# Optimization experiments

Measured on AMD Instinct MI355X. Metric: run time of the kernel, lower is better.

Reference implementation:

```python
import jax, jax.numpy as jnp
import numpy as np

H = 64  # hidden_size
B, S, DIN = 256, 4096, 1
NUM_LAYERS = 3


def setup_inputs() -> dict:
    key = jax.random.key(0)
    ks = jax.random.split(key, 32)
    s = 1.0 / np.sqrt(H)  # torch LSTM/Linear init bound
    inp = {"x": jax.random.normal(ks[0], (B, S, DIN), dtype=jnp.float32)}
    ki = 1
    for l in range(NUM_LAYERS):
        din = DIN if l == 0 else H
        inp[f"Wih{l}"] = jax.random.uniform(ks[ki], (4 * H, din), minval=-s, maxval=s); ki += 1
        inp[f"Whh{l}"] = jax.random.uniform(ks[ki], (4 * H, H), minval=-s, maxval=s); ki += 1
        inp[f"bih{l}"] = jax.random.uniform(ks[ki], (4 * H,), minval=-s, maxval=s); ki += 1
        inp[f"bhh{l}"] = jax.random.uniform(ks[ki], (4 * H,), minval=-s, maxval=s); ki += 1
    inp["Wlin"] = jax.random.uniform(ks[ki], (1, H), minval=-s, maxval=s); ki += 1
    inp["blin"] = jax.random.uniform(ks[ki], (1,), minval=-s, maxval=s)
    return inp


def _lstm_layer(x, Wih, Whh, bih, bhh):
    """x: [B,S,Din] -> (hs [B,S,H], h_T [B,H], c_T [B,H]). PyTorch gate order i,f,g,o."""
    # precompute input contribution for all timesteps (one big GEMM)
    xg = jnp.einsum('bsd,gd->bsg', x, Wih) + (bih + bhh)  # [B,S,4H]
    b = x.shape[0]
    h0 = jnp.zeros((b, H), x.dtype)
    c0 = jnp.zeros((b, H), x.dtype)

    def step(carry, xg_t):
        h, c = carry
        g = xg_t + h @ Whh.T  # [B,4H]
        i, f, gg, o = jnp.split(g, 4, axis=-1)
        c = jax.nn.sigmoid(f) * c + jax.nn.sigmoid(i) * jnp.tanh(gg)
        h = jax.nn.sigmoid(o) * jnp.tanh(c)
        return (h, c), h

    (hT, cT), hs = jax.lax.scan(step, (h0, c0), jnp.swapaxes(xg, 0, 1))
    return jnp.swapaxes(hs, 0, 1), hT, cT


def reference(x, Wih0, Whh0, bih0, bhh0, Wih1, Whh1, bih1, bhh1,
              Wih2, Whh2, bih2, bhh2, Wlin, blin):
    layers = [(Wih0, Whh0, bih0, bhh0), (Wih1, Whh1, bih1, bhh1), (Wih2, Whh2, bih2, bhh2)]
    out = x
    hTs, cTs = [], []
    for (Wih, Whh, bih, bhh) in layers:
        out, hT, cT = _lstm_layer(out, Wih, Whh, bih, bhh)
        hTs.append(hT); cTs.append(cT)
    y = out @ Wlin.T + blin  # [B,S,1]
    h_n = jnp.stack(hTs, axis=0)  # [num_layers,B,H]
    c_n = jnp.stack(cTs, axis=0)
    return y, h_n, c_n
```

## Files before the change

### kernel.cpp

```cpp
#include <hip/hip_runtime.h>
#include <stdint.h>


#define SQ 4096
#define HH 64
#define NB 256
#define WSEG 2048
#define WMAT 8192

typedef _Float16 h2  __attribute__((ext_vector_type(2)));
typedef uint32_t uv8 __attribute__((ext_vector_type(8)));

__device__ __forceinline__ h2 bch2(uint32_t u) { return __builtin_bit_cast(h2, u); }

template<int CTRL>
__device__ __forceinline__ float fdpp(float v) {
    return __builtin_bit_cast(float,
        __builtin_amdgcn_mov_dpp(__builtin_bit_cast(int, v), CTRL, 0xF, 0xF, true));
}
#define DPP_XOR1 0xB1
#define DPP_XOR2 0x4E
#define DPP_XOR3 0x1B
#define DPP_ROR4 0x124
#define DPP_ROR8 0x128

__device__ __forceinline__ float frcp(float x)  { return __builtin_amdgcn_rcpf(x); }
__device__ __forceinline__ float fexp2(float x) { return __builtin_amdgcn_exp2f(x); }

__device__ __forceinline__ uv8 load_pk(const uint32_t* __restrict__ p) {
    const uint4 a = *reinterpret_cast<const uint4*>(p);
    const uint4 b = *reinterpret_cast<const uint4*>(p + 4);
    uv8 r;
    r[0] = a.x; r[1] = a.y; r[2] = a.z; r[3] = a.w;
    r[4] = b.x; r[5] = b.y; r[6] = b.z; r[7] = b.w;
    return r;
}

__device__ __forceinline__ void pin(uv8& r) {
#pragma unroll
    for (int j = 0; j < 8; ++j) {
        uint32_t t = r[j];
        asm volatile("" : "+v"(t));
        r[j] = t;
    }
}

__device__ __forceinline__ float dotseg(uv8 w, uint4 a, uint4 b, float acc) {
    acc = __builtin_amdgcn_fdot2(bch2(w[0]), bch2(a.x), acc, false);
    acc = __builtin_amdgcn_fdot2(bch2(w[1]), bch2(a.y), acc, false);
    acc = __builtin_amdgcn_fdot2(bch2(w[2]), bch2(a.z), acc, false);
    acc = __builtin_amdgcn_fdot2(bch2(w[3]), bch2(a.w), acc, false);
    acc = __builtin_amdgcn_fdot2(bch2(w[4]), bch2(b.x), acc, false);
    acc = __builtin_amdgcn_fdot2(bch2(w[5]), bch2(b.y), acc, false);
    acc = __builtin_amdgcn_fdot2(bch2(w[6]), bch2(b.z), acc, false);
    acc = __builtin_amdgcn_fdot2(bch2(w[7]), bch2(b.w), acc, false);
    return acc;
}

__global__ __launch_bounds__(256)
void prep_weights(const float* __restrict__ Whh0, const float* __restrict__ Wih1,
                  const float* __restrict__ Whh1, const float* __restrict__ Wih2,
                  const float* __restrict__ Whh2, uint32_t* __restrict__ ws)
{
    const int idx = blockIdx.x * 256 + threadIdx.x;
    const int j   = idx & 7;
    const int k   = (idx >> 3) & 255;
    const int i   = (idx >> 11) & 3;
    const int mat = idx >> 13;
    const int u = k >> 2, qt = k & 3;
    const int row = ((qt ^ i) << 6) + u;
    const int col = (qt << 4) + (j << 1);
    const float* M = (mat == 0) ? Whh0 : (mat == 1) ? Wih1
                   : (mat == 2) ? Whh1 : (mat == 3) ? Wih2 : Whh2;
    h2 t;
    t[0] = (_Float16)M[row * HH + col];
    t[1] = (_Float16)M[row * HH + col + 1];
    ws[idx] = __builtin_bit_cast(uint32_t, t);
}

__global__ __launch_bounds__(768)
__attribute__((amdgpu_waves_per_eu(1, 3)))
void lstm3_fused(
    const float* __restrict__ x,
    const float* __restrict__ Wih0,
    const float* __restrict__ bih0, const float* __restrict__ bhh0,
    const float* __restrict__ bih1, const float* __restrict__ bhh1,
    const float* __restrict__ bih2, const float* __restrict__ bhh2,
    const float* __restrict__ Wlin, const float* __restrict__ blin,
    const uint32_t* __restrict__ wpk,
    float* __restrict__ out)
{
    const int b   = blockIdx.x;
    const int tid = threadIdx.x;
    const int grp = tid >> 8;
    const int k   = tid & 255;
    const int u   = k >> 2;
    const int qt  = k & 3;
    const int row = qt * HH + u;

    __shared__ __align__(16) float xrow[SQ];
    __shared__ __align__(16) uint4 hbf[2][3][8];
    __shared__ __align__(16) float ybuf[2][16];

    for (int i = tid; i < SQ; i += 768) xrow[i] = x[b * SQ + i];
    if (tid < 48) ((uint4*)hbf)[tid] = make_uint4(0, 0, 0, 0);
    if (tid < 32) ((float*)ybuf)[tid] = 0.f;

    const int matA = (grp == 0) ? 0 : (grp == 1) ? 1 : 3;
    const int matB = (grp == 1) ? 2 : 4;
    const uint32_t* pWA = wpk + matA * WMAT + k * 8;
    uv8 wA0 = load_pk(pWA + 0 * WSEG);
    uv8 wA1 = load_pk(pWA + 1 * WSEG);
    uv8 wA2 = load_pk(pWA + 2 * WSEG);
    uv8 wA3 = load_pk(pWA + 3 * WSEG);
    pin(wA0); pin(wA1); pin(wA2); pin(wA3);
    uv8 wB0 = {}, wB1 = {}, wB2 = {}, wB3 = {};
    if (grp != 0) {
        const uint32_t* pWB = wpk + matB * WMAT + k * 8;
        wB0 = load_pk(pWB + 0 * WSEG);
        wB1 = load_pk(pWB + 1 * WSEG);
        wB2 = load_pk(pWB + 2 * WSEG);
        wB3 = load_pk(pWB + 3 * WSEG);
        pin(wB0); pin(wB1); pin(wB2); pin(wB3);
    }

    float bias = 0.f, wih0 = 0.f, wlin_u = 0.f;
    if (grp == 0) { bias = bih0[row] + bhh0[row]; wih0 = Wih0[row]; }
    else if (grp == 1) bias = bih1[row] + bhh1[row];
    else { bias = bih2[row] + bhh2[row]; if (qt == 0) wlin_u = Wlin[u]; }
    const float blin_v = blin[0];

    const int la = (grp == 2) ? 1 : 0;
    const int lb = grp;
    const uint4* pA[2] = { &hbf[0][la][2 * qt], &hbf[1][la][2 * qt] };
    const uint4* pB[2] = { &hbf[0][lb][2 * qt], &hbf[1][lb][2 * qt] };
    _Float16* pW[2] = { (_Float16*)&hbf[0][grp][0] + u, (_Float16*)&hbf[1][grp][0] + u };

    const float s1  = (qt == 2) ? 2.f : 1.f;
    const float o1  = (qt == 2) ? 1.f : 0.f;
    const float ms1 = -s1 * 1.44269504f;
    float cc = 0.f;

    __syncthreads();

    auto tick = [&](int T, int rd) {
        const int wr = rd ^ 1;

        const uint4 a0 = pA[rd][0], a1 = pA[rd][1];
        float p0 = dotseg(wA0, a0, a1, 0.f);
        float p1 = dotseg(wA1, a0, a1, 0.f);
        float p2 = dotseg(wA2, a0, a1, 0.f);
        float p3 = dotseg(wA3, a0, a1, 0.f);
        if (grp != 0) {
            const uint4 c0 = pB[rd][0], c1 = pB[rd][1];
            p0 = dotseg(wB0, c0, c1, p0);
            p1 = dotseg(wB1, c0, c1, p1);
            p2 = dotseg(wB2, c0, c1, p2);
            p3 = dotseg(wB3, c0, c1, p3);
        }

        float g = (p0 + fdpp<DPP_XOR1>(p1))
                + fdpp<DPP_XOR2>(p2 + fdpp<DPP_XOR1>(p3));
        g += bias;
        if (grp == 0) g += wih0 * xrow[(T < SQ) ? T : 0];

        const float t   = frcp(1.f + fexp2(ms1 * g));
        const float act = s1 * t - o1;
        const float v1 = fdpp<DPP_XOR1>(act);
        const float v2 = fdpp<DPP_XOR2>(act);
        const float v3 = fdpp<DPP_XOR3>(act);

        const int step = T - grp;
        float yv = 0.f;
        if (qt == 0 && step >= 0 && step < SQ) {
            cc = v1 * cc + act * v2;
            float tc = fminf(fmaxf(cc, -15.f), 15.f);
            float e  = fexp2(tc * -2.88539008f);
            float h  = v3 * ((1.f - e) * frcp(1.f + e));
            *pW[wr] = (_Float16)h;
            if (grp == 2) yv = wlin_u * h;
            if (step == SQ - 1) {
                out[NB * SQ + grp * NB * HH + b * HH + u] = h;
                out[NB * SQ + 3 * NB * HH + grp * NB * HH + b * HH + u] = cc;
            }
        }
        if (grp == 2) {
            yv += fdpp<DPP_XOR1>(yv);
            yv += fdpp<DPP_XOR2>(yv);
            yv += fdpp<DPP_ROR4>(yv);
            yv += fdpp<DPP_ROR8>(yv);
            if ((k & 15) == 0) ybuf[rd][k >> 4] = yv;
        }
        if (grp == 0 && u == HH - 1) {
            const int sy = T - 3;
            if (sy >= 0 && sy < SQ) {
                const float4 v = ((const float4*)ybuf[rd ^ 1])[qt];
                float s = (v.x + v.y) + (v.z + v.w);
                s += fdpp<DPP_XOR1>(s);
                s += fdpp<DPP_XOR2>(s);
                if (qt == 3) out[b * SQ + sy] = s + blin_v;
            }
        }
        __syncthreads();
    };

    for (int T = 0; T < SQ + 4; T += 2) {
        tick(T, 0);
        tick(T + 1, 1);
    }
}

extern "C" void kernel_launch(void* const* d_in, const int* in_sizes, int n_in,
                              void* d_out, int out_size, void* d_ws, size_t ws_size,
                              hipStream_t stream) {
    const float* x    = (const float*)d_in[0];
    const float* Wih0 = (const float*)d_in[1];
    const float* Whh0 = (const float*)d_in[2];
    const float* bih0 = (const float*)d_in[3];
    const float* bhh0 = (const float*)d_in[4];
    const float* Wih1 = (const float*)d_in[5];
    const float* Whh1 = (const float*)d_in[6];
    const float* bih1 = (const float*)d_in[7];
    const float* bhh1 = (const float*)d_in[8];
    const float* Wih2 = (const float*)d_in[9];
    const float* Whh2 = (const float*)d_in[10];
    const float* bih2 = (const float*)d_in[11];
    const float* bhh2 = (const float*)d_in[12];
    const float* Wlin = (const float*)d_in[13];
    const float* blin = (const float*)d_in[14];
    float* out = (float*)d_out;

    uint32_t* wpk = (uint32_t*)d_ws;
    prep_weights<<<160, 256, 0, stream>>>(Whh0, Wih1, Whh1, Wih2, Whh2, wpk);
    lstm3_fused<<<NB, 768, 0, stream>>>(x, Wih0, bih0, bhh0,
                                        bih1, bhh1, bih2, bhh2,
                                        Wlin, blin, wpk, out);
}
```

Before: 2.894 ms.

## Compute recurrent LSTM matvecs with MFMA 16x16x32 instead of fdot2 chains

Replaces the per-lane fdot2 dot-product chains and DPP cross-lane gate reduction with MFMA 16x16x32 f16 instructions. The weights are repacked into MFMA A-fragment layout, and the h vector is broadcast as the B operand, so only one output column is meaningful. Results are scattered to a new LDS gate buffer by one lane per 16, then read back per gate row. This trades many VALU dot instructions for matrix-core ops plus an extra LDS round trip on the per-step critical path. It also wastes 15 of the 16 MFMA columns.

```diff
diff --git a/kernel.cpp b/kernel.cpp
--- a/kernel.cpp
+++ b/kernel.cpp
@@ -5,13 +5,10 @@
 #define SQ 4096
 #define HH 64
 #define NB 256
-#define WSEG 2048
-#define WMAT 8192
-
-typedef _Float16 h2  __attribute__((ext_vector_type(2)));
-typedef uint32_t uv8 __attribute__((ext_vector_type(8)));
-
-__device__ __forceinline__ h2 bch2(uint32_t u) { return __builtin_bit_cast(h2, u); }
+
+typedef _Float16 h2    __attribute__((ext_vector_type(2)));
+typedef _Float16 f16x8 __attribute__((ext_vector_type(8)));
+typedef float    f32x4 __attribute__((ext_vector_type(4)));
 
 template<int CTRL>
 __device__ __forceinline__ float fdpp(float v) {
@@ -27,34 +24,13 @@
 __device__ __forceinline__ float frcp(float x)  { return __builtin_amdgcn_rcpf(x); }
 __device__ __forceinline__ float fexp2(float x) { return __builtin_amdgcn_exp2f(x); }
 
-__device__ __forceinline__ uv8 load_pk(const uint32_t* __restrict__ p) {
-    const uint4 a = *reinterpret_cast<const uint4*>(p);
-    const uint4 b = *reinterpret_cast<const uint4*>(p + 4);
-    uv8 r;
-    r[0] = a.x; r[1] = a.y; r[2] = a.z; r[3] = a.w;
-    r[4] = b.x; r[5] = b.y; r[6] = b.z; r[7] = b.w;
-    return r;
-}
-
-__device__ __forceinline__ void pin(uv8& r) {
-#pragma unroll
-    for (int j = 0; j < 8; ++j) {
-        uint32_t t = r[j];
-        asm volatile("" : "+v"(t));
-        r[j] = t;
-    }
-}
-
-__device__ __forceinline__ float dotseg(uv8 w, uint4 a, uint4 b, float acc) {
-    acc = __builtin_amdgcn_fdot2(bch2(w[0]), bch2(a.x), acc, false);
-    acc = __builtin_amdgcn_fdot2(bch2(w[1]), bch2(a.y), acc, false);
-    acc = __builtin_amdgcn_fdot2(bch2(w[2]), bch2(a.z), acc, false);
-    acc = __builtin_amdgcn_fdot2(bch2(w[3]), bch2(a.w), acc, false);
-    acc = __builtin_amdgcn_fdot2(bch2(w[4]), bch2(b.x), acc, false);
-    acc = __builtin_amdgcn_fdot2(bch2(w[5]), bch2(b.y), acc, false);
-    acc = __builtin_amdgcn_fdot2(bch2(w[6]), bch2(b.z), acc, false);
-    acc = __builtin_amdgcn_fdot2(bch2(w[7]), bch2(b.w), acc, false);
-    return acc;
+__device__ __forceinline__ void pin4(uint4& r) {
+    asm volatile("" : "+v"(r.x), "+v"(r.y), "+v"(r.z), "+v"(r.w));
+}
+
+__device__ __forceinline__ f32x4 mm(uint4 wv, uint4 bv, f32x4 c) {
+    return __builtin_amdgcn_mfma_f32_16x16x32_f16(
+        __builtin_bit_cast(f16x8, wv), __builtin_bit_cast(f16x8, bv), c, 0, 0, 0);
 }
 
 __global__ __launch_bounds__(256)
@@ -63,19 +39,29 @@
                   const float* __restrict__ Whh2, uint32_t* __restrict__ ws)
 {
     const int idx = blockIdx.x * 256 + threadIdx.x;
-    const int j   = idx & 7;
-    const int k   = (idx >> 3) & 255;
-    const int i   = (idx >> 11) & 3;
-    const int mat = idx >> 13;
-    const int u = k >> 2, qt = k & 3;
-    const int row = ((qt ^ i) << 6) + u;
-    const int col = (qt << 4) + (j << 1);
-    const float* M = (mat == 0) ? Whh0 : (mat == 1) ? Wih1
-                   : (mat == 2) ? Whh1 : (mat == 3) ? Wih2 : Whh2;
-    h2 t;
-    t[0] = (_Float16)M[row * HH + col];
-    t[1] = (_Float16)M[row * HH + col + 1];
-    ws[idx] = __builtin_bit_cast(uint32_t, t);
+    int r, KT;
+    const float *Wi = nullptr, *Wh;
+    if (idx < 8192)       { r = idx;         KT = 2; Wh = Whh0; }
+    else if (idx < 24576) { r = idx - 8192;  KT = 4; Wi = Wih1; Wh = Whh1; }
+    else                  { r = idx - 24576; KT = 4; Wi = Wih2; Wh = Whh2; }
+    const int j   = r & 3;
+    const int l   = (r >> 2) & 63;
+    const int rem = r >> 8;
+    const int kt  = rem & (KT - 1);
+    const int tw  = rem / KT;
+    const int t   = tw & 3;
+    const int w   = tw >> 2;
+    const int p    = w * 64 + t * 16 + (l & 15);
+    const int orow = (p & 3) * 64 + (p >> 2);
+    const int kk   = (l >> 4) * 8 + 2 * j;
+    const float* M; int col;
+    if (KT == 2)     { M = Wh; col = kt * 32 + kk; }
+    else if (kt < 2) { M = Wi; col = kt * 32 + kk; }
+    else             { M = Wh; col = (kt - 2) * 32 + kk; }
+    h2 tt;
+    tt[0] = (_Float16)M[orow * HH + col];
+    tt[1] = (_Float16)M[orow * HH + col + 1];
+    ws[idx] = __builtin_bit_cast(uint32_t, tt);
 }
 
 __global__ __launch_bounds__(768)
@@ -97,31 +83,38 @@
     const int u   = k >> 2;
     const int qt  = k & 3;
     const int row = qt * HH + u;
+    const int w   = k >> 6;
+    const int l   = k & 63;
+    const int q   = l >> 4;
+    const bool lz = (l & 15) == 0;
 
     __shared__ __align__(16) float xrow[SQ];
     __shared__ __align__(16) uint4 hbf[2][3][8];
     __shared__ __align__(16) float ybuf[2][16];
+    __shared__ __align__(16) float gbuf[3][256];
 
     for (int i = tid; i < SQ; i += 768) xrow[i] = x[b * SQ + i];
     if (tid < 48) ((uint4*)hbf)[tid] = make_uint4(0, 0, 0, 0);
     if (tid < 32) ((float*)ybuf)[tid] = 0.f;
 
-    const int matA = (grp == 0) ? 0 : (grp == 1) ? 1 : 3;
-    const int matB = (grp == 1) ? 2 : 4;
-    const uint32_t* pWA = wpk + matA * WMAT + k * 8;
-    uv8 wA0 = load_pk(pWA + 0 * WSEG);
-    uv8 wA1 = load_pk(pWA + 1 * WSEG);
-    uv8 wA2 = load_pk(pWA + 2 * WSEG);
-    uv8 wA3 = load_pk(pWA + 3 * WSEG);
-    pin(wA0); pin(wA1); pin(wA2); pin(wA3);
-    uv8 wB0 = {}, wB1 = {}, wB2 = {}, wB3 = {};
+    const int gbase = (grp == 0) ? 0 : (grp == 1) ? 8192 : 24576;
+    const int KT    = (grp == 0) ? 2 : 4;
+    const uint32_t* wbp = wpk + gbase;
+    auto fr = [&](int t_, int kt_) {
+        return *reinterpret_cast<const uint4*>(
+            wbp + (((w * 4 + t_) * KT + kt_) * 64 + l) * 4);
+    };
+    uint4 w00 = fr(0, 0), w01 = fr(0, 1), w10 = fr(1, 0), w11 = fr(1, 1),
+          w20 = fr(2, 0), w21 = fr(2, 1), w30 = fr(3, 0), w31 = fr(3, 1);
+    pin4(w00); pin4(w01); pin4(w10); pin4(w11);
+    pin4(w20); pin4(w21); pin4(w30); pin4(w31);
+    uint4 w02 = {}, w03 = {}, w12 = {}, w13 = {},
+          w22 = {}, w23 = {}, w32 = {}, w33 = {};
     if (grp != 0) {
-        const uint32_t* pWB = wpk + matB * WMAT + k * 8;
-        wB0 = load_pk(pWB + 0 * WSEG);
-        wB1 = load_pk(pWB + 1 * WSEG);
-        wB2 = load_pk(pWB + 2 * WSEG);
-        wB3 = load_pk(pWB + 3 * WSEG);
-        pin(wB0); pin(wB1); pin(wB2); pin(wB3);
+        w02 = fr(0, 2); w03 = fr(0, 3); w12 = fr(1, 2); w13 = fr(1, 3);
+        w22 = fr(2, 2); w23 = fr(2, 3); w32 = fr(3, 2); w33 = fr(3, 3);
+        pin4(w02); pin4(w03); pin4(w12); pin4(w13);
+        pin4(w22); pin4(w23); pin4(w32); pin4(w33);
     }
 
     float bias = 0.f, wih0 = 0.f, wlin_u = 0.f;
@@ -132,8 +125,8 @@
 
     const int la = (grp == 2) ? 1 : 0;
     const int lb = grp;
-    const uint4* pA[2] = { &hbf[0][la][2 * qt], &hbf[1][la][2 * qt] };
-    const uint4* pB[2] = { &hbf[0][lb][2 * qt], &hbf[1][lb][2 * qt] };
+    const uint4* pA[2] = { &hbf[0][la][0], &hbf[1][la][0] };
+    const uint4* pB[2] = { &hbf[0][lb][0], &hbf[1][lb][0] };
     _Float16* pW[2] = { (_Float16*)&hbf[0][grp][0] + u, (_Float16*)&hbf[1][grp][0] + u };
 
     const float s1  = (qt == 2) ? 2.f : 1.f;
@@ -141,27 +134,36 @@
     const float ms1 = -s1 * 1.44269504f;
     float cc = 0.f;
 
+    const f32x4 Z = {0.f, 0.f, 0.f, 0.f};
+
     __syncthreads();
 
     auto tick = [&](int T, int rd) {
         const int wr = rd ^ 1;
 
-        const uint4 a0 = pA[rd][0], a1 = pA[rd][1];
-        float p0 = dotseg(wA0, a0, a1, 0.f);
-        float p1 = dotseg(wA1, a0, a1, 0.f);
-        float p2 = dotseg(wA2, a0, a1, 0.f);
-        float p3 = dotseg(wA3, a0, a1, 0.f);
+        const uint4* hA = pA[rd];
+        const uint4 b0 = hA[q], b1 = hA[4 + q];
+        f32x4 d0 = mm(w00, b0, Z);  f32x4 d1 = mm(w10, b0, Z);
+        f32x4 d2 = mm(w20, b0, Z);  f32x4 d3 = mm(w30, b0, Z);
+        d0 = mm(w01, b1, d0);  d1 = mm(w11, b1, d1);
+        d2 = mm(w21, b1, d2);  d3 = mm(w31, b1, d3);
         if (grp != 0) {
-            const uint4 c0 = pB[rd][0], c1 = pB[rd][1];
-            p0 = dotseg(wB0, c0, c1, p0);
-            p1 = dotseg(wB1, c0, c1, p1);
-            p2 = dotseg(wB2, c0, c1, p2);
-            p3 = dotseg(wB3, c0, c1, p3);
-        }
-
-        float g = (p0 + fdpp<DPP_XOR1>(p1))
-                + fdpp<DPP_XOR2>(p2 + fdpp<DPP_XOR1>(p3));
-        g += bias;
+            const uint4* hB = pB[rd];
+            const uint4 b2 = hB[q], b3 = hB[4 + q];
+            d0 = mm(w02, b2, d0);  d1 = mm(w12, b2, d1);
+            d2 = mm(w22, b2, d2);  d3 = mm(w32, b2, d3);
+            d0 = mm(w03, b3, d0);  d1 = mm(w13, b3, d1);
+            d2 = mm(w23, b3, d2);  d3 = mm(w33, b3, d3);
+        }
+
+        if (lz) {
+            float* gb = &gbuf[grp][w * 64 + 4 * q];
+            *reinterpret_cast<f32x4*>(gb)      = d0;
+            *reinterpret_cast<f32x4*>(gb + 16) = d1;
+            *reinterpret_cast<f32x4*>(gb + 32) = d2;
+            *reinterpret_cast<f32x4*>(gb + 48) = d3;
+        }
+        float g = gbuf[grp][k] + bias;
         if (grp == 0) g += wih0 * xrow[(T < SQ) ? T : 0];
 
         const float t   = frcp(1.f + fexp2(ms1 * g));
```

New measurement: 3.140 ms. 8.5% more time.
